# Optimization experiments

Hardware: AMD Instinct MI355X
Metric: run time of the kernel (lower is better)

## Reference

```python
import jax, jax.numpy as jnp
import numpy as np

EPS = 1e-12

def _l2norm(x):
    # F.normalize(p=2, dim=1) with eps clamp on the norm
    n = jnp.linalg.norm(x, axis=1, keepdims=True)
    return x / jnp.maximum(n, EPS)

def _xavier_uniform(key, shape, gain=1.414):
    fan_in, fan_out = shape[-1], shape[0]
    a = gain * np.sqrt(6.0 / (fan_in + fan_out))
    return jax.random.uniform(key, shape, jnp.float32, -a, a)

def setup_inputs() -> dict:
    NUM_ENT, NUM_REL, D, E, B = 100000, 500, 512, 150000, 4096
    key = jax.random.key(0)
    ks = jax.random.split(key, 12)
    heads = jax.random.randint(ks[0], (B, 1), 0, NUM_ENT)
    rels  = jax.random.randint(ks[1], (B, 1), 0, NUM_REL)
    tails = jax.random.randint(ks[2], (B, 1), 0, NUM_ENT)
    triples = jnp.concatenate([heads, rels, tails], axis=1)           # [B,3]
    node_list = jax.random.randint(ks[3], (2, E), 0, NUM_ENT)          # [2,E] (src,dst)
    edge_list = jax.random.randint(ks[4], (E,), 0, NUM_REL)            # [E] relation per edge
    return {
        "triples": triples,
        "node_list": node_list,
        "edge_list": edge_list,
        "ent_emb_init": jax.random.normal(ks[5], (NUM_ENT, D), jnp.float32),
        "rel_emb_init": jax.random.normal(ks[6], (NUM_REL, D), jnp.float32),
        "W_1": _xavier_uniform(ks[7], (D, D)),
        "W_a": _xavier_uniform(ks[8], (1, D)),
        "g_0": _xavier_uniform(ks[9], (1, D)),
        "W_E": _xavier_uniform(ks[10], (D, D)),
        "W_R": _xavier_uniform(ks[11], (D, D)),
    }

def reference(triples, node_list, edge_list, ent_emb_init, rel_emb_init,
              W_1, W_a, g_0, W_E, W_R):
    num_ent = ent_emb_init.shape[0]
    e0 = _l2norm(ent_emb_init)                      # normalized entity table [N,D]
    src, dst = node_list[0], node_list[1]
    h_i = e0[src]                                   # [E,D]
    h_j = e0[dst]                                   # [E,D]
    g_k = rel_emb_init[edge_list]                   # [E,D]

    # c_ijk = W_1 @ (h_j*g_k)^T  -> kept edge-major as [E,D]
    c = (h_j * g_k) @ W_1.T                         # [E,D]
    a = -jax.nn.leaky_relu((h_i * jnp.tanh(c)) @ W_a[0], 0.2)   # [E]
    c_base = (h_i * g_0) @ W_1.T                    # [E,D]
    a_base = -jax.nn.leaky_relu((h_i * jnp.tanh(c_base)) @ W_a[0], 0.2)  # [E]

    a_exp = jnp.exp(a)                              # [E]
    ab_exp = jnp.exp(a_base)                        # [E]

    # segment-softmax denominator: sum of edge exps per source node + baseline term
    a_exp_sum = jax.ops.segment_sum(a_exp[:, None], src, num_segments=num_ent)  # [N,1]
    # baseline exp depends only on src node -> duplicate scatter-set writes identical values
    ab_sorted = jnp.zeros_like(a_exp_sum).at[src].set(ab_exp[:, None])           # [N,1]
    denom = ab_sorted + a_exp_sum
    denom = jnp.where(denom == 0.0, EPS, denom)

    # weighted scatter-aggregate of messages (dropout omitted: eval-mode identity)
    ac = a_exp[:, None] * c                         # [E,D]
    ac_base = ab_exp[:, None] * c_base              # [E,D]
    a_new = jax.ops.segment_sum(ac, src, num_segments=num_ent)                   # [N,D]
    ab_new = jnp.zeros_like(a_new).at[src].set(ac_base)                          # [N,D]

    h_prime = jax.nn.elu((ab_new + a_new) / denom)  # [N,D]
    ent_new = _l2norm(e0 @ W_E + h_prime)           # [N,D]
    rel_new = rel_emb_init @ W_R                    # [R,D]

    head = ent_new[triples[:, 0]][:, None, :]       # [B,1,D]
    rel  = rel_new[triples[:, 1]][:, None, :]       # [B,1,D]
    tail = ent_new[triples[:, 2]][:, None, :]       # [B,1,D]
    return jnp.concatenate([head, rel, tail], axis=1)  # [B,3,D]
```

## Files before the change

kernel.cpp:

```cpp
#include <hip/hip_runtime.h>
#include <cmath>


#define DDIM 512
#define MAXM 65536
#define GBM 128
#define GBN 128

typedef __attribute__((ext_vector_type(8))) short short8;
typedef __attribute__((ext_vector_type(4))) short short4v;
typedef __attribute__((ext_vector_type(4))) float fv4;
typedef unsigned short u16;
typedef unsigned long long u64;

__device__ __forceinline__ float elu1(float x) { return x > 0.f ? x : expm1f(x); }
__device__ __forceinline__ float sexp(float x) {
    float lr = x >= 0.f ? x : 0.2f * x;
    return expf(-lr);
}
__device__ __forceinline__ u16 f2bf(float x) {
    unsigned u = __float_as_uint(x);
    u += 0x7FFFu + ((u >> 16) & 1u);
    return (u16)(u >> 16);
}
__device__ __forceinline__ float bf2f(u16 h) {
    return __uint_as_float((unsigned)h << 16);
}
__device__ __forceinline__ void cvt8(const float* v, short8& h8, short8& l8) {
    #pragma unroll
    for (int i = 0; i < 8; i++) {
        u16 h = f2bf(v[i]);
        h8[i] = (short)h;
        l8[i] = (short)f2bf(v[i] - bf2f(h));
    }
}
__device__ __forceinline__ void gld16(const void* g, void* l) {
    __builtin_amdgcn_global_load_lds(
        (const __attribute__((address_space(1))) unsigned int*)g,
        (__attribute__((address_space(3))) unsigned int*)l,
        16, 0, 0);
}

__global__ void hist_kernel(const int* __restrict__ src, int* __restrict__ cnt, int E)
{
    int e = blockIdx.x * 256 + threadIdx.x;
    if (e < E) atomicAdd(&cnt[src[e]], 1);
}

__global__ __launch_bounds__(1024)
void scan_lookback_kernel(const int* __restrict__ in, int* __restrict__ out,
                          int* __restrict__ out2, int n,
                          int* __restrict__ ticket, u64* __restrict__ state)
{
    __shared__ int sh[1024];
    __shared__ int bidSh, exSh;
    int t = threadIdx.x;
    if (t == 0) bidSh = atomicAdd(ticket, 1);
    __syncthreads();
    int bid = bidSh;
    int i = bid * 1024 + t;
    int v = (i < n) ? in[i] : 0;
    sh[t] = v;
    __syncthreads();
    for (int o = 1; o < 1024; o <<= 1) {
        int x = (t >= o) ? sh[t - o] : 0;
        __syncthreads();
        sh[t] += x;
        __syncthreads();
    }
    int incl = sh[t];
    int agg = sh[1023];
    if (t == 0) {
        u64 pub = (bid == 0) ? ((2ull << 32) | (unsigned)agg)
                             : ((1ull << 32) | (unsigned)agg);
        __hip_atomic_store(&state[bid], pub, __ATOMIC_RELEASE, __HIP_MEMORY_SCOPE_AGENT);
        int ex = 0;
        if (bid > 0) {
            int p = bid - 1;
            for (;;) {
                u64 s;
                do {
                    s = __hip_atomic_load(&state[p], __ATOMIC_ACQUIRE, __HIP_MEMORY_SCOPE_AGENT);
                } while ((s >> 32) == 0);
                ex += (int)(unsigned)s;
                if ((s >> 32) == 2ull) break;
                p--;
            }
            __hip_atomic_store(&state[bid], (2ull << 32) | (unsigned)(ex + agg),
                               __ATOMIC_RELEASE, __HIP_MEMORY_SCOPE_AGENT);
        }
        exSh = ex;
    }
    __syncthreads();
    int ex = exSh;
    if (i < n) {
        int e = ex + incl - v;
        out[i] = e;
        if (out2) out2[i] = e;
        if (i == n - 1) out[n] = ex + incl;
    }
}

__global__ __launch_bounds__(1024)
void scan_small_kernel(const int* __restrict__ in, int* __restrict__ out, int n)
{
    __shared__ int sh[1024];
    __shared__ int carrySh;
    int t = threadIdx.x;
    if (t == 0) carrySh = 0;
    __syncthreads();
    for (int base = 0; base < n; base += 1024) {
        int i = base + t;
        int v = (i < n) ? in[i] : 0;
        sh[t] = v;
        __syncthreads();
        for (int o = 1; o < 1024; o <<= 1) {
            int x = (t >= o) ? sh[t - o] : 0;
            __syncthreads();
            sh[t] += x;
            __syncthreads();
        }
        int carry = carrySh;
        if (i < n) out[i] = carry + sh[t] - v;
        __syncthreads();
        if (t == 1023) carrySh = carry + sh[1023];
        __syncthreads();
    }
    if (t == 0) out[n] = carrySh;
}

__global__ void bucket_slotdeg_kernel(const int* __restrict__ src, int* __restrict__ cursor,
                                      int* __restrict__ edge_ids, int E,
                                      const int* __restrict__ triples, const int* __restrict__ rowSt,
                                      int* __restrict__ slotNode, int* __restrict__ deg, int NS)
{
    int i = blockIdx.x * 256 + threadIdx.x;
    if (i < E) { int p = atomicAdd(&cursor[src[i]], 1); edge_ids[p] = i; }
    int r = i - E;
    if (r >= 0 && r < NS) {
        int b = r >> 1, p = (r & 1) * 2;
        int n = triples[b * 3 + p];
        slotNode[r] = n;
        deg[r] = rowSt[n + 1] - rowSt[n];
    }
}

__global__ void fill_rows_kernel(const int* __restrict__ slotNode, const int* __restrict__ rowSt,
                                 const int* __restrict__ edgeIds, const int* __restrict__ slotOff,
                                 int* __restrict__ rows, int* __restrict__ srcL, int NS)
{
    int r = blockIdx.x * 256 + threadIdx.x;
    if (r >= NS) return;
    int n = slotNode[r];
    int gs = rowSt[n], d = rowSt[n + 1] - gs, mo = slotOff[r];
    for (int j = 0; j < d && mo + j < MAXM; j++) {
        rows[mo + j] = edgeIds[gs + j];
        srcL[mo + j] = n;
    }
}


__global__ __launch_bounds__(256)
void wfrag_kernel(const float* __restrict__ W1, const float* __restrict__ WE,
                  const float* __restrict__ WR, const float* __restrict__ relEmb,
                  int R,
                  u16* __restrict__ W1H, u16* __restrict__ W1L,
                  u16* __restrict__ WEH, u16* __restrict__ WEL,
                  u16* __restrict__ WRH, u16* __restrict__ WRL,
                  u16* __restrict__ ArH, u16* __restrict__ ArL)
{
    int mat = blockIdx.y;
    const float* src = (mat == 0) ? W1 : (mat == 1) ? WE : (mat == 2) ? WR : relEmb;
    u16* hi = (mat == 0) ? W1H : (mat == 1) ? WEH : (mat == 2) ? WRH : ArH;
    u16* lo = (mat == 0) ? W1L : (mat == 1) ? WEL : (mat == 2) ? WRL : ArL;
    bool tr = (mat == 1 || mat == 2);
    int rows = (mat == 3) ? R : DDIM;

    int nt = ((rows + 127) >> 7) << 3;
    int wid = threadIdx.x >> 6, lane = threadIdx.x & 63;
    int l15 = lane & 15, seg = (lane >> 4) * 8;
    for (int rt = blockIdx.x * 4 + wid; rt < nt; rt += gridDim.x * 4) {
        int r = min(rt * 16 + l15, rows - 1);
        size_t base = (size_t)rt * 8192 + (size_t)lane * 8;
        #pragma unroll 2
        for (int kt = 0; kt < 16; kt++) {
            float v[8];
            if (!tr) {
                const float* p = src + (size_t)r * DDIM + seg + kt * 32;
                float4 x0 = *(const float4*)p;
                float4 x1 = *(const float4*)(p + 4);
                v[0]=x0.x; v[1]=x0.y; v[2]=x0.z; v[3]=x0.w;
                v[4]=x1.x; v[5]=x1.y; v[6]=x1.z; v[7]=x1.w;
            } else {
                int k0 = kt * 32 + seg;
                #pragma unroll
                for (int i = 0; i < 8; i++)
                    v[i] = src[(size_t)(k0 + i) * DDIM + r];
            }
            short8 h8, l8; cvt8(v, h8, l8);
            *(short8*)(hi + base + (size_t)kt * 512) = h8;
            *(short8*)(lo + base + (size_t)kt * 512) = l8;
        }
    }
}

__global__ __launch_bounds__(256)
void afrag_es_kernel(const float* __restrict__ entEmb, float* __restrict__ invN,
                     const float* __restrict__ relEmb, const float* __restrict__ g0,
                     const int* __restrict__ rowsL, const int* __restrict__ dstIdx,
                     const int* __restrict__ relIdx, const int* __restrict__ slotNode,
                     const int* __restrict__ Mdev, int NS,
                     u16* __restrict__ AeH, u16* __restrict__ AeL,
                     u16* __restrict__ As1H, u16* __restrict__ As1L,
                     u16* __restrict__ As3H, u16* __restrict__ As3L)
{
    int M = max(1, min(MAXM, *Mdev));
    int ntE = ((M + 127) >> 7) << 3;
    int ntS = ((NS + 127) >> 7) << 3;
    int total = ntE + ntS;
    int wid = threadIdx.x >> 6, lane = threadIdx.x & 63;
    int l15 = lane & 15, seg = (lane >> 4) * 8;

    for (int g = blockIdx.x * 4 + wid; g < total; g += gridDim.x * 4) {
        bool isE = g < ntE;
        int rt = isE ? g : g - ntE;
        int node, rl = 0;
        if (isE) {
            int m = min(rt * 16 + l15, M - 1);
            int e = rowsL[m];
            node = dstIdx[e]; rl = relIdx[e];
        } else {
            node = slotNode[min(rt * 16 + l15, NS - 1)];
        }
        const float* ep = entEmb + (size_t)node * DDIM + seg;
        float ss = 0.f;
        for (int kt = 0; kt < 16; kt++) {
            float4 x0 = *(const float4*)(ep + kt * 32);
            float4 x1 = *(const float4*)(ep + kt * 32 + 4);
            ss += x0.x*x0.x + x0.y*x0.y + x0.z*x0.z + x0.w*x0.w
                + x1.x*x1.x + x1.y*x1.y + x1.z*x1.z + x1.w*x1.w;
        }
        ss += __shfl_xor(ss, 16);
        ss += __shfl_xor(ss, 32);
        float sc = 1.f / fmaxf(sqrtf(ss), 1e-12f);
        if (lane < 16) invN[node] = sc;
        size_t base = (size_t)rt * 8192 + (size_t)lane * 8;
        if (isE) {
            const float* rp = relEmb + (size_t)rl * DDIM + seg;
            #pragma unroll 4
            for (int kt = 0; kt < 16; kt++) {
                float4 x0 = *(const float4*)(ep + kt * 32);
                float4 x1 = *(const float4*)(ep + kt * 32 + 4);
                float4 y0 = *(const float4*)(rp + kt * 32);
                float4 y1 = *(const float4*)(rp + kt * 32 + 4);
                float v[8] = {sc*x0.x*y0.x, sc*x0.y*y0.y, sc*x0.z*y0.z, sc*x0.w*y0.w,
                              sc*x1.x*y1.x, sc*x1.y*y1.y, sc*x1.z*y1.z, sc*x1.w*y1.w};
                short8 h8, l8; cvt8(v, h8, l8);
                *(short8*)(AeH + base + (size_t)kt * 512) = h8;
                *(short8*)(AeL + base + (size_t)kt * 512) = l8;
            }
        } else {
            const float* gp = g0 + seg;
            #pragma unroll 2
            for (int kt = 0; kt < 16; kt++) {
                float4 x0 = *(const float4*)(ep + kt * 32);
                float4 x1 = *(const float4*)(ep + kt * 32 + 4);
                float4 y0 = *(const float4*)(gp + kt * 32);
                float4 y1 = *(const float4*)(gp + kt * 32 + 4);
                float v3[8] = {sc*x0.x, sc*x0.y, sc*x0.z, sc*x0.w,
                               sc*x1.x, sc*x1.y, sc*x1.z, sc*x1.w};
                float v1[8] = {v3[0]*y0.x, v3[1]*y0.y, v3[2]*y0.z, v3[3]*y0.w,
                               v3[4]*y1.x, v3[5]*y1.y, v3[6]*y1.z, v3[7]*y1.w};
                short8 h8, l8;
                cvt8(v3, h8, l8);
                *(short8*)(As3H + base + (size_t)kt * 512) = h8;
                *(short8*)(As3L + base + (size_t)kt * 512) = l8;
                cvt8(v1, h8, l8);
                *(short8*)(As1H + base + (size_t)kt * 512) = h8;
                *(short8*)(As1L + base + (size_t)kt * 512) = l8;
            }
        }
    }
}

__global__ __launch_bounds__(256)
void gemm_score_k(const u16* __restrict__ AeH, const u16* __restrict__ AeL,
                  const u16* __restrict__ As1H, const u16* __restrict__ As1L,
                  const u16* __restrict__ W1H, const u16* __restrict__ W1L,
                  const float* __restrict__ entEmb, const float* __restrict__ invNorm,
                  const int* __restrict__ srcL, const int* __restrict__ slotNode,
                  const float* __restrict__ Wa, float* __restrict__ scoreP,
                  const int* __restrict__ Mdev, int NS, int SCLEN)
{
    __shared__ __align__(1024) u16 lds[2][32 * 512];
    int M = max(1, min(MAXM, *Mdev));
    int TE = (M + 127) >> 7, TS = (NS + 127) >> 7;
    int total = TE + TS;
    int lane = threadIdx.x & 63, wid = threadIdx.x >> 6;
    int waveM = wid >> 1, waveN = wid & 1;
    int quad = lane >> 4, l15 = lane & 15;
    int n0 = blockIdx.y * GBN;
    int ldsChunk0 = wid * 8;

    for (int tt = blockIdx.x; tt < total; tt += gridDim.x) {
        bool isE = tt < TE;
        int m0 = (isE ? tt : tt - TE) * GBM;
        int Mt = isE ? M : NS;
        const u16* g1 = isE
            ? ((wid == 0) ? AeH : (wid == 1) ? AeL : (wid == 2) ? W1H : W1L)
            : ((wid == 0) ? As1H : (wid == 1) ? As1L : (wid == 2) ? W1H : W1L);
        int rowBase = (wid < 2) ? (m0 >> 4) : (n0 >> 4);
        const u16* s1 = g1 + (size_t)rowBase * 8192 + (size_t)lane * 8;

        fv4 acc[4][4];
        #pragma unroll
        for (int i = 0; i < 4; i++)
            #pragma unroll
            for (int j = 0; j < 4; j++) acc[i][j] = fv4{0.f, 0.f, 0.f, 0.f};

        int cur = 0;
        #pragma unroll
        for (int q = 0; q < 8; q++)
            gld16(s1 + (size_t)q * 8192, &lds[0][(ldsChunk0 + q) * 512]);
        __syncthreads();

        for (int kk = 0; kk < 16; kk++) {
            if (kk < 15) {
                size_t go = (size_t)(kk + 1) * 512;
                #pragma unroll
                for (int q = 0; q < 8; q++)
                    gld16(s1 + (size_t)q * 8192 + go,
                          &lds[cur ^ 1][(ldsChunk0 + q) * 512]);
            }
            const u16* buf = &lds[cur][0];
            short8 aH[4], aL[4], bH[4], bL[4];
            #pragma unroll
            for (int i = 0; i < 4; i++) {
                aH[i] = *(const short8*)&buf[(waveM * 4 + i) * 512 + lane * 8];
                aL[i] = *(const short8*)&buf[(8 + waveM * 4 + i) * 512 + lane * 8];
                bH[i] = *(const short8*)&buf[(16 + waveN * 4 + i) * 512 + lane * 8];
                bL[i] = *(const short8*)&buf[(24 + waveN * 4 + i) * 512 + lane * 8];
            }
            #pragma unroll
            for (int i = 0; i < 4; i++)
                #pragma unroll
                for (int j = 0; j < 4; j++) {
                    acc[i][j] = __builtin_amdgcn_mfma_f32_16x16x32_bf16(aH[i], bH[j], acc[i][j], 0, 0, 0);
                    acc[i][j] = __builtin_amdgcn_mfma_f32_16x16x32_bf16(aH[i], bL[j], acc[i][j], 0, 0, 0);
                    acc[i][j] = __builtin_amdgcn_mfma_f32_16x16x32_bf16(aL[i], bH[j], acc[i][j], 0, 0, 0);
                }
            __syncthreads();
            cur ^= 1;
        }

        int base = isE ? 0 : MAXM;
        #pragma unroll
        for (int i = 0; i < 4; i++) {
            #pragma unroll
            for (int reg = 0; reg < 4; reg++) {
                int gm = m0 + waveM * 64 + i * 16 + quad * 4 + reg;
                bool valid = gm < Mt;
                int gmc = valid ? gm : 0;
                int srcn = isE ? srcL[gmc] : slotNode[gmc];
                float invs = invNorm[srcn];
                float s = 0.f;
                #pragma unroll
                for (int j = 0; j < 4; j++) {
                    int col = n0 + waveN * 64 + j * 16 + l15;
                    float hv = entEmb[(size_t)srcn * DDIM + col];
                    float wv = Wa[col];
                    s += tanhf(acc[i][j][reg]) * hv * wv;
                }
                s *= invs;
                s += __shfl_xor(s, 8); s += __shfl_xor(s, 4);
                s += __shfl_xor(s, 2); s += __shfl_xor(s, 1);
                if (l15 == 0 && valid)
                    scoreP[(size_t)blockIdx.y * SCLEN + base + gm] = s;
            }
        }
    }
}

__global__ __launch_bounds__(256)
void gemm_tail_k(const u16* __restrict__ ApH, const u16* __restrict__ ApL,
                 const u16* __restrict__ W1H, const u16* __restrict__ W1L,
                 const u16* __restrict__ As3H, const u16* __restrict__ As3L,
                 const u16* __restrict__ WEH, const u16* __restrict__ WEL,
                 const u16* __restrict__ ArH, const u16* __restrict__ ArL,
                 const u16* __restrict__ WRH, const u16* __restrict__ WRL,
                 const float* __restrict__ invDenom,
                 float* __restrict__ ENT, float* __restrict__ relnew, int NS, int R)
{
    __shared__ __align__(1024) u16 lds[2][32 * 512];
    int lane = threadIdx.x & 63, wid = threadIdx.x >> 6;
    int waveM = wid >> 1, waveN = wid & 1;
    int quad = lane >> 4, l15 = lane & 15;
    int n0 = blockIdx.y * GBN;
    int TS = (NS + 127) >> 7, TR = (R + 127) >> 7;
    int total = TS + TR;
    int ldsChunk0 = wid * 8;

    for (int tt = blockIdx.x; tt < total; tt += gridDim.x) {
        bool fused = tt < TS;
        int m0 = (fused ? tt : tt - TS) * GBM;
        int Mt = fused ? NS : R;
        float* Cout = fused ? ENT : relnew;
        const u16* g1 = fused
            ? ((wid == 0) ? ApH : (wid == 1) ? ApL : (wid == 2) ? W1H : W1L)
            : ((wid == 0) ? ArH : (wid == 1) ? ArL : (wid == 2) ? WRH : WRL);
        const u16* g2 = fused
            ? ((wid == 0) ? As3H : (wid == 1) ? As3L : (wid == 2) ? WEH : WEL)
            : nullptr;
        int nkk = fused ? 32 : 16;
        int rowBase = (wid < 2) ? (m0 >> 4) : (n0 >> 4);
        const u16* s1 = g1 + (size_t)rowBase * 8192 + (size_t)lane * 8;
        const u16* s2 = fused ? g2 + (size_t)rowBase * 8192 + (size_t)lane * 8 : nullptr;

        fv4 acc[4][4];
        #pragma unroll
        for (int i = 0; i < 4; i++)
            #pragma unroll
            for (int j = 0; j < 4; j++) acc[i][j] = fv4{0.f, 0.f, 0.f, 0.f};

        int cur = 0;
        #pragma unroll
        for (int q = 0; q < 8; q++)
            gld16(s1 + (size_t)q * 8192, &lds[0][(ldsChunk0 + q) * 512]);
        __syncthreads();

        for (int kk = 0; kk < nkk; kk++) {
            int kn = kk + 1;
            if (kn < nkk) {
                const u16* sp = (fused && kn >= 16) ? s2 : s1;
                size_t go = (size_t)(kn & 15) * 512;
                #pragma unroll
                for (int q = 0; q < 8; q++)
                    gld16(sp + (size_t)q * 8192 + go,
                          &lds[cur ^ 1][(ldsChunk0 + q) * 512]);
            }
            const u16* buf = &lds[cur][0];
            short8 aH[4], aL[4], bH[4], bL[4];
            #pragma unroll
            for (int i = 0; i < 4; i++) {
                aH[i] = *(const short8*)&buf[(waveM * 4 + i) * 512 + lane * 8];
                aL[i] = *(const short8*)&buf[(8 + waveM * 4 + i) * 512 + lane * 8];
                bH[i] = *(const short8*)&buf[(16 + waveN * 4 + i) * 512 + lane * 8];
                bL[i] = *(const short8*)&buf[(24 + waveN * 4 + i) * 512 + lane * 8];
            }
            #pragma unroll
            for (int i = 0; i < 4; i++)
                #pragma unroll
                for (int j = 0; j < 4; j++) {
                    acc[i][j] = __builtin_amdgcn_mfma_f32_16x16x32_bf16(aH[i], bH[j], acc[i][j], 0, 0, 0);
                    acc[i][j] = __builtin_amdgcn_mfma_f32_16x16x32_bf16(aH[i], bL[j], acc[i][j], 0, 0, 0);
                    acc[i][j] = __builtin_amdgcn_mfma_f32_16x16x32_bf16(aL[i], bH[j], acc[i][j], 0, 0, 0);
                }
            if (fused && kk == 15) {
                #pragma unroll
                for (int i = 0; i < 4; i++)
                    #pragma unroll
                    for (int reg = 0; reg < 4; reg++) {
                        int gm = m0 + waveM * 64 + i * 16 + quad * 4 + reg;
                        float idv = invDenom[min(gm, Mt - 1)];
                        #pragma unroll
                        for (int j = 0; j < 4; j++)
                            acc[i][j][reg] = elu1(acc[i][j][reg] * idv);
                    }
            }
            __syncthreads();
            cur ^= 1;
        }

        #pragma unroll
        for (int i = 0; i < 4; i++) {
            #pragma unroll
            for (int reg = 0; reg < 4; reg++) {
                int gm = m0 + waveM * 64 + i * 16 + quad * 4 + reg;
                if (gm >= Mt) continue;
                #pragma unroll
                for (int j = 0; j < 4; j++) {
                    int col = n0 + waveN * 64 + j * 16 + l15;
                    Cout[(size_t)gm * DDIM + col] = acc[i][j][reg];
                }
            }
        }
    }
}

__global__ __launch_bounds__(128)
void build_p_kernel(const float* __restrict__ entEmb, const float* __restrict__ invNorm,
                    const float* __restrict__ relEmb, const float* __restrict__ g0,
                    const int* __restrict__ slotNode, const int* __restrict__ rowSt,
                    const int* __restrict__ edgeIds, const int* __restrict__ dstIdx,
                    const int* __restrict__ relIdx, const int* __restrict__ slotOff,
                    const float* __restrict__ scoreP, int SCLEN, int NS,
                    u16* __restrict__ ApH, u16* __restrict__ ApL,
                    float* __restrict__ invDenom)
{
    int r = blockIdx.x, t = threadIdx.x;
    float4 acc = make_float4(0.f, 0.f, 0.f, 0.f);
    float dInv = 1.f;
    if (r < NS) {
        int n = slotNode[r];
        int gs = rowSt[n], d = rowSt[n + 1] - gs;
        if (d > 0) {
            int mo = slotOff[r];
            int si = MAXM + r;
            float ab = sexp(scoreP[si] + scoreP[SCLEN + si]
                          + scoreP[2 * SCLEN + si] + scoreP[3 * SCLEN + si]);
            float sc = ab * invNorm[n];
            float4 ev = *(const float4*)(entEmb + (size_t)n * DDIM + t * 4);
            float4 gv = *(const float4*)(g0 + t * 4);
            acc = make_float4(sc*ev.x*gv.x, sc*ev.y*gv.y, sc*ev.z*gv.z, sc*ev.w*gv.w);
            float denom = ab;
            for (int j = 0; j < d; j++) {
                if (mo + j >= MAXM) break;
                int e = edgeIds[gs + j];
                int ei = mo + j;
                float ae = sexp(scoreP[ei] + scoreP[SCLEN + ei]
                              + scoreP[2 * SCLEN + ei] + scoreP[3 * SCLEN + ei]);
                int dn = dstIdx[e], rl = relIdx[e];
                float s = ae * invNorm[dn];
                float4 dv = *(const float4*)(entEmb + (size_t)dn * DDIM + t * 4);
                float4 rv = *(const float4*)(relEmb + (size_t)rl * DDIM + t * 4);
                acc.x = fmaf(s, dv.x*rv.x, acc.x);
                acc.y = fmaf(s, dv.y*rv.y, acc.y);
                acc.z = fmaf(s, dv.z*rv.z, acc.z);
                acc.w = fmaf(s, dv.w*rv.w, acc.w);
                denom += ae;
            }
            dInv = 1.f / denom;
        }
    }
    int kt = t >> 3;
    int lane = (r & 15) + 16 * ((t >> 1) & 3);
    int j0 = (t & 1) * 4;
    size_t fo = (size_t)(r >> 4) * 8192 + (size_t)kt * 512 + (size_t)lane * 8 + j0;
    float v[4] = {acc.x, acc.y, acc.z, acc.w};
    short4v h4, l4;
    #pragma unroll
    for (int i = 0; i < 4; i++) {
        u16 h = f2bf(v[i]);
        h4[i] = (short)h;
        l4[i] = (short)f2bf(v[i] - bf2f(h));
    }
    *(short4v*)(ApH + fo) = h4;
    *(short4v*)(ApL + fo) = l4;
    if (t == 0 && r < NS) invDenom[r] = dInv;
}

__global__ __launch_bounds__(128)
void gather_out_kernel(const int* __restrict__ triples, const float* __restrict__ ENT,
                       const float* __restrict__ relnew, float* __restrict__ out)
{
    int r = blockIdx.x;
    int b = r / 3, j = r - b * 3;
    int t = threadIdx.x;
    size_t oo = (size_t)r * DDIM + t * 4;
    if (j == 1) {
        const float* srow = relnew + (size_t)triples[r] * DDIM;
        *(float4*)(out + oo) = *(const float4*)(srow + t * 4);
        return;
    }
    const float* srow = ENT + (size_t)(b * 2 + (j == 2 ? 1 : 0)) * DDIM;
    float4 v = *(const float4*)(srow + t * 4);
    float s = v.x*v.x + v.y*v.y + v.z*v.z + v.w*v.w;
    #pragma unroll
    for (int off = 32; off > 0; off >>= 1) s += __shfl_down(s, off);
    __shared__ float ws2[2];
    if ((t & 63) == 0) ws2[t >> 6] = s;
    __syncthreads();
    float inv = 1.f / fmaxf(sqrtf(ws2[0] + ws2[1]), 1e-12f);
    *(float4*)(out + oo) = make_float4(v.x*inv, v.y*inv, v.z*inv, v.w*inv);
}

extern "C" void kernel_launch(void* const* d_in, const int* in_sizes, int n_in,
                              void* d_out, int out_size, void* d_ws, size_t ws_size,
                              hipStream_t stream)
{
    const int*   triples = (const int*)  d_in[0];
    const int*   nodes   = (const int*)  d_in[1];
    const int*   edges   = (const int*)  d_in[2];
    const float* entEmb  = (const float*)d_in[3];
    const float* relEmb  = (const float*)d_in[4];
    const float* W1      = (const float*)d_in[5];
    const float* Wa      = (const float*)d_in[6];
    const float* g0      = (const float*)d_in[7];
    const float* WE      = (const float*)d_in[8];
    const float* WR      = (const float*)d_in[9];

    const int B  = in_sizes[0] / 3;
    const int E  = in_sizes[2];
    const int N  = in_sizes[3] / DDIM;
    const int R  = in_sizes[4] / DDIM;
    const int NS = 2 * B;
    const int* srcIdx = nodes;
    const int* dstIdx = nodes + E;

    char* ws = (char*)d_ws;
    size_t off = 0;
    auto carve = [&](size_t bytes) -> void* {
        void* p = ws + off;
        off = (off + bytes + 255) & ~(size_t)255;
        return p;
    };
    const int NS128 = ((NS + 127) / 128) * 128;
    const int R128  = ((R + 127) / 128) * 128;
    const int SCLEN = MAXM + NS128;
    float* ENT      = (float*)carve((size_t)NS * DDIM * 4);
    float* relnew   = (float*)carve((size_t)R * DDIM * 4);
    float* invNorm  = (float*)carve((size_t)N * 4);
    float* scoreP   = (float*)carve((size_t)4 * SCLEN * 4);
    float* invDen   = (float*)carve((size_t)NS * 4);
    char*  zbase    = ws + off;
    int*   cnt      = (int*)carve((size_t)N * 4);
    int*   ticket   = (int*)carve(256);
    u64*   stateN   = (u64*)carve((size_t)1024 * 8);
    size_t zbytes   = (size_t)((ws + off) - zbase);
    int*   rowSt    = (int*)carve((size_t)(N + 1) * 4);
    int*   cursor   = (int*)carve((size_t)N * 4);
    int*   edgeIds  = (int*)carve((size_t)E * 4);
    int*   slotNode = (int*)carve((size_t)NS * 4);
    int*   deg      = (int*)carve((size_t)NS * 4);
    int*   slotOff  = (int*)carve((size_t)(NS + 1) * 4);
    int*   rowsL    = (int*)carve((size_t)MAXM * 4);
    int*   srcL     = (int*)carve((size_t)MAXM * 4);
    u16* AeH  = (u16*)carve((size_t)MAXM * DDIM * 2);
    u16* AeL  = (u16*)carve((size_t)MAXM * DDIM * 2);
    u16* As1H = (u16*)carve((size_t)NS128 * DDIM * 2);
    u16* As1L = (u16*)carve((size_t)NS128 * DDIM * 2);
    u16* As3H = (u16*)carve((size_t)NS128 * DDIM * 2);
    u16* As3L = (u16*)carve((size_t)NS128 * DDIM * 2);
    u16* ApH  = (u16*)carve((size_t)NS128 * DDIM * 2);
    u16* ApL  = (u16*)carve((size_t)NS128 * DDIM * 2);
    u16* ArH  = (u16*)carve((size_t)R128 * DDIM * 2);
    u16* ArL  = (u16*)carve((size_t)R128 * DDIM * 2);
    u16* W1H  = (u16*)carve((size_t)DDIM * DDIM * 2);
    u16* W1L  = (u16*)carve((size_t)DDIM * DDIM * 2);
    u16* WEH  = (u16*)carve((size_t)DDIM * DDIM * 2);
    u16* WEL  = (u16*)carve((size_t)DDIM * DDIM * 2);
    u16* WRH  = (u16*)carve((size_t)DDIM * DDIM * 2);
    u16* WRL  = (u16*)carve((size_t)DDIM * DDIM * 2);
    (void)ws_size; (void)n_in; (void)out_size;

    hipMemsetAsync(zbase, 0, zbytes, stream);
    hist_kernel<<<(E + 255) / 256, 256, 0, stream>>>(srcIdx, cnt, E);
    scan_lookback_kernel<<<(N + 1023) / 1024, 1024, 0, stream>>>(
        cnt, rowSt, cursor, N, ticket, stateN);
    bucket_slotdeg_kernel<<<(E + NS + 255) / 256, 256, 0, stream>>>(
        srcIdx, cursor, edgeIds, E, triples, rowSt, slotNode, deg, NS);
    scan_small_kernel<<<1, 1024, 0, stream>>>(deg, slotOff, NS);
    const int* Mdev = slotOff + NS;
    fill_rows_kernel<<<(NS + 255) / 256, 256, 0, stream>>>(slotNode, rowSt, edgeIds,
                                                           slotOff, rowsL, srcL, NS);
    wfrag_kernel<<<dim3(8, 4), 256, 0, stream>>>(W1, WE, WR, relEmb, R,
                                                 W1H, W1L, WEH, WEL, WRH, WRL, ArH, ArL);
    afrag_es_kernel<<<256, 256, 0, stream>>>(entEmb, invNorm, relEmb, g0,
                                             rowsL, dstIdx, edges, slotNode,
                                             Mdev, NS,
                                             AeH, AeL, As1H, As1L, As3H, As3L);
    gemm_score_k<<<dim3(192, DDIM / GBN), 256, 0, stream>>>(
        AeH, AeL, As1H, As1L, W1H, W1L, entEmb, invNorm, srcL, slotNode,
        Wa, scoreP, Mdev, NS, SCLEN);
    build_p_kernel<<<NS128, 128, 0, stream>>>(entEmb, invNorm, relEmb, g0, slotNode,
                                              rowSt, edgeIds, dstIdx, edges, slotOff,
                                              scoreP, SCLEN, NS, ApH, ApL, invDen);
    int gTail = ((NS + GBM - 1) / GBM) + ((R + GBM - 1) / GBM);
    gemm_tail_k<<<dim3(gTail, DDIM / GBN), 256, 0, stream>>>(
        ApH, ApL, W1H, W1L, As3H, As3L, WEH, WEL, ArH, ArL, WRH, WRL,
        invDen, ENT, relnew, NS, R);
    gather_out_kernel<<<B * 3, 128, 0, stream>>>(triples, ENT, relnew, (float*)d_out);
}
```

Measured before the change: 500.5 us.

## Reuse packed A fragments in build_p, use fast tanh/elu, shuffle scan, occupancy hints

build_p_kernel now rebuilds its aggregate from the already computed bf16 hi/lo A-fragment buffers (AeH/AeL, As1H/As1L). It no longer re-gathers entity and relation rows and re-multiplies them, which cuts random global gathers per edge. tanhf and expm1f are replaced with exp2/rcp intrinsic versions, the small scan uses wave shuffles instead of a barrier-heavy LDS scan, and the GEMM kernels get a min-blocks-per-CU launch hint. Risks are small precision loss from the split-bf16 reconstruction and fast math, and possible register spills from the occupancy hint.

```diff
diff --git a/kernel.cpp b/kernel.cpp
--- a/kernel.cpp
+++ b/kernel.cpp
@@ -13,7 +13,16 @@
 typedef unsigned short u16;
 typedef unsigned long long u64;
 
-__device__ __forceinline__ float elu1(float x) { return x > 0.f ? x : expm1f(x); }
+#define LOG2E 1.4426950408889634f
+
+__device__ __forceinline__ float fast_tanh(float x) {
+    x = fminf(fmaxf(x, -30.f), 30.f);
+    float e = __builtin_amdgcn_exp2f(2.f * LOG2E * x);
+    return (e - 1.f) * __builtin_amdgcn_rcpf(e + 1.f);
+}
+__device__ __forceinline__ float fast_elu(float x) {
+    return x > 0.f ? x : (__builtin_amdgcn_exp2f(LOG2E * x) - 1.f);
+}
 __device__ __forceinline__ float sexp(float x) {
     float lr = x >= 0.f ? x : 0.2f * x;
     return expf(-lr);
@@ -104,26 +113,28 @@
 __global__ __launch_bounds__(1024)
 void scan_small_kernel(const int* __restrict__ in, int* __restrict__ out, int n)
 {
-    __shared__ int sh[1024];
+    __shared__ int wsum[16];
     __shared__ int carrySh;
-    int t = threadIdx.x;
+    int t = threadIdx.x, lane = t & 63, w = t >> 6;
     if (t == 0) carrySh = 0;
     __syncthreads();
     for (int base = 0; base < n; base += 1024) {
         int i = base + t;
         int v = (i < n) ? in[i] : 0;
-        sh[t] = v;
+        int s = v;
+        #pragma unroll
+        for (int o = 1; o < 64; o <<= 1) {
+            int x = __shfl_up(s, o);
+            if (lane >= o) s += x;
+        }
+        if (lane == 63) wsum[w] = s;
         __syncthreads();
-        for (int o = 1; o < 1024; o <<= 1) {
-            int x = (t >= o) ? sh[t - o] : 0;
-            __syncthreads();
-            sh[t] += x;
-            __syncthreads();
-        }
+        int wo = 0;
+        for (int k = 0; k < w; k++) wo += wsum[k];
         int carry = carrySh;
-        if (i < n) out[i] = carry + sh[t] - v;
+        if (i < n) out[i] = carry + wo + s - v;
         __syncthreads();
-        if (t == 1023) carrySh = carry + sh[1023];
+        if (t == 1023) carrySh = carry + wo + s;
         __syncthreads();
     }
     if (t == 0) out[n] = carrySh;
@@ -283,7 +294,7 @@
     }
 }
 
-__global__ __launch_bounds__(256)
+__global__ __launch_bounds__(256, 2)
 void gemm_score_k(const u16* __restrict__ AeH, const u16* __restrict__ AeL,
                   const u16* __restrict__ As1H, const u16* __restrict__ As1L,
                   const u16* __restrict__ W1H, const u16* __restrict__ W1L,
@@ -369,7 +380,7 @@
                     int col = n0 + waveN * 64 + j * 16 + l15;
                     float hv = entEmb[(size_t)srcn * DDIM + col];
                     float wv = Wa[col];
-                    s += tanhf(acc[i][j][reg]) * hv * wv;
+                    s += fast_tanh(acc[i][j][reg]) * hv * wv;
                 }
                 s *= invs;
                 s += __shfl_xor(s, 8); s += __shfl_xor(s, 4);
@@ -381,7 +392,7 @@
     }
 }
 
-__global__ __launch_bounds__(256)
+__global__ __launch_bounds__(256, 2)
 void gemm_tail_k(const u16* __restrict__ ApH, const u16* __restrict__ ApL,
                  const u16* __restrict__ W1H, const u16* __restrict__ W1L,
                  const u16* __restrict__ As3H, const u16* __restrict__ As3L,
@@ -464,7 +475,7 @@
                         float idv = invDenom[min(gm, Mt - 1)];
                         #pragma unroll
                         for (int j = 0; j < 4; j++)
-                            acc[i][j][reg] = elu1(acc[i][j][reg] * idv);
+                            acc[i][j][reg] = fast_elu(acc[i][j][reg] * idv);
                     }
             }
             __syncthreads();
@@ -488,55 +499,54 @@
 }
 
 __global__ __launch_bounds__(128)
-void build_p_kernel(const float* __restrict__ entEmb, const float* __restrict__ invNorm,
-                    const float* __restrict__ relEmb, const float* __restrict__ g0,
-                    const int* __restrict__ slotNode, const int* __restrict__ rowSt,
-                    const int* __restrict__ edgeIds, const int* __restrict__ dstIdx,
-                    const int* __restrict__ relIdx, const int* __restrict__ slotOff,
+void build_p_kernel(const int* __restrict__ deg, const int* __restrict__ slotOff,
                     const float* __restrict__ scoreP, int SCLEN, int NS,
+                    const u16* __restrict__ AeH, const u16* __restrict__ AeL,
+                    const u16* __restrict__ As1H, const u16* __restrict__ As1L,
                     u16* __restrict__ ApH, u16* __restrict__ ApL,
                     float* __restrict__ invDenom)
 {
     int r = blockIdx.x, t = threadIdx.x;
-    float4 acc = make_float4(0.f, 0.f, 0.f, 0.f);
+    int kt = t >> 3;
+    int qsel = (t >> 1) & 3;
+    int j0 = (t & 1) * 4;
+    size_t ktoff = (size_t)kt * 512 + j0;
+    float a0 = 0.f, a1 = 0.f, a2 = 0.f, a3 = 0.f;
     float dInv = 1.f;
     if (r < NS) {
-        int n = slotNode[r];
-        int gs = rowSt[n], d = rowSt[n + 1] - gs;
+        int d = deg[r];
         if (d > 0) {
             int mo = slotOff[r];
             int si = MAXM + r;
             float ab = sexp(scoreP[si] + scoreP[SCLEN + si]
                           + scoreP[2 * SCLEN + si] + scoreP[3 * SCLEN + si]);
-            float sc = ab * invNorm[n];
-            float4 ev = *(const float4*)(entEmb + (size_t)n * DDIM + t * 4);
-            float4 gv = *(const float4*)(g0 + t * 4);
-            acc = make_float4(sc*ev.x*gv.x, sc*ev.y*gv.y, sc*ev.z*gv.z, sc*ev.w*gv.w);
+            size_t so = (size_t)(r >> 4) * 8192 + ktoff + (size_t)((r & 15) + 16 * qsel) * 8;
+            short4v h4 = *(const short4v*)(As1H + so);
+            short4v l4 = *(const short4v*)(As1L + so);
+            a0 = ab * (bf2f((u16)h4[0]) + bf2f((u16)l4[0]));
+            a1 = ab * (bf2f((u16)h4[1]) + bf2f((u16)l4[1]));
+            a2 = ab * (bf2f((u16)h4[2]) + bf2f((u16)l4[2]));
+            a3 = ab * (bf2f((u16)h4[3]) + bf2f((u16)l4[3]));
             float denom = ab;
             for (int j = 0; j < d; j++) {
-                if (mo + j >= MAXM) break;
-                int e = edgeIds[gs + j];
                 int ei = mo + j;
+                if (ei >= MAXM) break;
                 float ae = sexp(scoreP[ei] + scoreP[SCLEN + ei]
                               + scoreP[2 * SCLEN + ei] + scoreP[3 * SCLEN + ei]);
-                int dn = dstIdx[e], rl = relIdx[e];
-                float s = ae * invNorm[dn];
-                float4 dv = *(const float4*)(entEmb + (size_t)dn * DDIM + t * 4);
-                float4 rv = *(const float4*)(relEmb + (size_t)rl * DDIM + t * 4);
-                acc.x = fmaf(s, dv.x*rv.x, acc.x);
-                acc.y = fmaf(s, dv.y*rv.y, acc.y);
-                acc.z = fmaf(s, dv.z*rv.z, acc.z);
-                acc.w = fmaf(s, dv.w*rv.w, acc.w);
+                size_t eo = (size_t)(ei >> 4) * 8192 + ktoff + (size_t)((ei & 15) + 16 * qsel) * 8;
+                short4v eh = *(const short4v*)(AeH + eo);
+                short4v el = *(const short4v*)(AeL + eo);
+                a0 = fmaf(ae, bf2f((u16)eh[0]) + bf2f((u16)el[0]), a0);
+                a1 = fmaf(ae, bf2f((u16)eh[1]) + bf2f((u16)el[1]), a1);
+                a2 = fmaf(ae, bf2f((u16)eh[2]) + bf2f((u16)el[2]), a2);
+                a3 = fmaf(ae, bf2f((u16)eh[3]) + bf2f((u16)el[3]), a3);
                 denom += ae;
             }
             dInv = 1.f / denom;
         }
     }
-    int kt = t >> 3;
-    int lane = (r & 15) + 16 * ((t >> 1) & 3);
-    int j0 = (t & 1) * 4;
-    size_t fo = (size_t)(r >> 4) * 8192 + (size_t)kt * 512 + (size_t)lane * 8 + j0;
-    float v[4] = {acc.x, acc.y, acc.z, acc.w};
+    size_t fo = (size_t)(r >> 4) * 8192 + ktoff + (size_t)((r & 15) + 16 * qsel) * 8;
+    float v[4] = {a0, a1, a2, a3};
     short4v h4, l4;
     #pragma unroll
     for (int i = 0; i < 4; i++) {
@@ -662,9 +672,9 @@
     gemm_score_k<<<dim3(192, DDIM / GBN), 256, 0, stream>>>(
         AeH, AeL, As1H, As1L, W1H, W1L, entEmb, invNorm, srcL, slotNode,
         Wa, scoreP, Mdev, NS, SCLEN);
-    build_p_kernel<<<NS128, 128, 0, stream>>>(entEmb, invNorm, relEmb, g0, slotNode,
-                                              rowSt, edgeIds, dstIdx, edges, slotOff,
-                                              scoreP, SCLEN, NS, ApH, ApL, invDen);
+    build_p_kernel<<<NS128, 128, 0, stream>>>(deg, slotOff, scoreP, SCLEN, NS,
+                                              AeH, AeL, As1H, As1L,
+                                              ApH, ApL, invDen);
     int gTail = ((NS + GBM - 1) / GBM) + ((R + GBM - 1) / GBM);
     gemm_tail_k<<<dim3(gTail, DDIM / GBN), 256, 0, stream>>>(
         ApH, ApL, W1H, W1L, As3H, As3L, WEH, WEL, ArH, ArL, WRH, WRL,
```

Result: no change. 503.1 us (+0.5%).
